# Optimization experiments

Measured on AMD Instinct MI355X. Metric: run time of the kernel, lower is better.

The kernel has to match this reference:

```python
import jax, jax.numpy as jnp
import numpy as np

WIDTH = 4096
DEPTH = 512
N_HIST = 20
N_SCALES = 64
BIAS_SCALE = 1.0


def setup_inputs() -> dict:
    key = jax.random.key(0)
    k1, k2, k3, k4, k5 = jax.random.split(key, 5)
    x = jax.random.normal(k1, (WIDTH,), dtype=jnp.float32)
    biases = jax.random.normal(k2, (DEPTH, WIDTH), dtype=jnp.float32)
    W = jax.random.normal(k3, (WIDTH, WIDTH), dtype=jnp.float32)          # linop.Random matrix
    W_bias = jax.random.normal(k4, (WIDTH, WIDTH), dtype=jnp.float32)
    weight_scales = jax.random.uniform(k5, (N_SCALES,), dtype=jnp.float32)
    return {"x": x, "biases": biases, "W": W, "W_bias": W_bias,
            "weight_scales": weight_scales}


def reference(x, biases, W, W_bias, weight_scales):
    """forward_parallel of Network (mode='rand', no residual, no normalize).

    Returns (n_scales, n_hist, width): last n_hist states of a depth-unrolled
    reservoir: curr <- erf(s * (curr @ W^T) + bias) / sqrt(width).
    """
    inv_sqrt_w = np.float32(1.0 / np.sqrt(WIDTH))
    # biases = einsum('ij,nj->ni', W_bias, biases): (depth, width)
    b = jnp.einsum('ij,nj->ni', W_bias, biases)
    curr0 = jnp.tile(x[None, :], (N_SCALES, 1))  # (n_scales, width)

    def step(curr, bi):
        pre = weight_scales[:, None] * (curr @ W.T) + BIAS_SCALE * bi[None, :]
        nxt = jax.scipy.special.erf(pre) * inv_sqrt_w
        return nxt, nxt

    _, states = jax.lax.scan(step, curr0, b)       # (depth, n_scales, width)
    out = jnp.transpose(states[-N_HIST:], (1, 0, 2))  # (n_scales, n_hist, width)
    return out
```

## Files before the change

### kernel.cpp

```cpp
#include <hip/hip_runtime.h>
#include <cstdint>
#include <cstddef>

#define WIDTH 4096
#define DEPTH 512
#define NHIST 20
#define NWG 256
#define NTHR 1024

typedef __attribute__((ext_vector_type(4))) float f32x4;
typedef __attribute__((ext_vector_type(8))) short bf16x8;

__device__ __forceinline__ ushort f2bf(float f) {
    uint32_t u = __float_as_uint(f);
    u += 0x7FFFu + ((u >> 16) & 1u);
    return (ushort)(u >> 16);
}


__global__ __launch_bounds__(256) void init_curr_kernel(const float* __restrict__ x,
                                                        ushort* __restrict__ cur) {
    int g = blockIdx.x * 256 + threadIdx.x;
    int kv = g >> 6, m = g & 63;
    int unit = ((kv >> 2) * 4 + (m >> 4)) * 64 + (kv & 3) * 16 + (m & 15);
    ushort4 lo, hi;
    lo.x = f2bf(x[kv * 8 + 0]); lo.y = f2bf(x[kv * 8 + 1]);
    lo.z = f2bf(x[kv * 8 + 2]); lo.w = f2bf(x[kv * 8 + 3]);
    hi.x = f2bf(x[kv * 8 + 4]); hi.y = f2bf(x[kv * 8 + 5]);
    hi.z = f2bf(x[kv * 8 + 6]); hi.w = f2bf(x[kv * 8 + 7]);
    ushort* dst = cur + (size_t)unit * 8;
    *(ushort4*)dst = lo;
    *(ushort4*)(dst + 4) = hi;
}

__global__ __launch_bounds__(256) void zero_flags_kernel(int* __restrict__ flags) {
    flags[blockIdx.x * 256 + threadIdx.x] = 0;
}

__global__ __launch_bounds__(256) void bias_gemm_kernel(const float* __restrict__ A,
                                                        const float* __restrict__ B,
                                                        float* __restrict__ C) {
    __shared__ float As[64][36];
    __shared__ float Bs[64][36];
    const int bm = blockIdx.y;
    const int bn = blockIdx.x;
    const int t  = threadIdx.x;
    const int tx = t & 15, ty = t >> 4;
    const int lr = t >> 3;
    const int lc = (t & 7) * 4;

    float acc[4][4] = {};
    for (int k0 = 0; k0 < WIDTH; k0 += 32) {
        float4 a0 = *(const float4*)&A[(size_t)(bm * 64 + lr) * WIDTH + k0 + lc];
        float4 a1 = *(const float4*)&A[(size_t)(bm * 64 + lr + 32) * WIDTH + k0 + lc];
        float4 b0 = *(const float4*)&B[(size_t)(bn * 64 + lr) * WIDTH + k0 + lc];
        float4 b1 = *(const float4*)&B[(size_t)(bn * 64 + lr + 32) * WIDTH + k0 + lc];
        __syncthreads();
        *(float4*)&As[lr][lc] = a0;  *(float4*)&As[lr + 32][lc] = a1;
        *(float4*)&Bs[lr][lc] = b0;  *(float4*)&Bs[lr + 32][lc] = b1;
        __syncthreads();
        #pragma unroll
        for (int k = 0; k < 32; k += 4) {
            float4 av[4], bv[4];
            #pragma unroll
            for (int mi = 0; mi < 4; mi++) av[mi] = *(const float4*)&As[ty * 4 + mi][k];
            #pragma unroll
            for (int ni = 0; ni < 4; ni++) bv[ni] = *(const float4*)&Bs[tx * 4 + ni][k];
            #pragma unroll
            for (int mi = 0; mi < 4; mi++)
                #pragma unroll
                for (int ni = 0; ni < 4; ni++)
                    acc[mi][ni] += av[mi].x * bv[ni].x + av[mi].y * bv[ni].y +
                                   av[mi].z * bv[ni].z + av[mi].w * bv[ni].w;
        }
    }
    #pragma unroll
    for (int mi = 0; mi < 4; mi++) {
        float4 v = make_float4(acc[mi][0], acc[mi][1], acc[mi][2], acc[mi][3]);
        *(float4*)&C[(size_t)(bm * 64 + ty * 4 + mi) * WIDTH + bn * 64 + tx * 4] = v;
    }
}

__global__ __launch_bounds__(NTHR, 4) void reservoir_kernel(
    const float* __restrict__ W,
    const float* __restrict__ scales,
    const float* __restrict__ b,
    float* __restrict__ out,
    ushort* __restrict__ cur0,
    ushort* __restrict__ cur1,
    int* __restrict__ flags)
{
    __shared__ float partial[16 * 32 * 32];
    __shared__ float vals[32 * 33];

    const int tid  = threadIdx.x;
    const int w    = tid >> 6;
    const int lane = tid & 63;
    const int lrow = lane & 15;
    const int lq   = lane >> 4;
    const int t    = blockIdx.x;
    const int c0   = (t >> 1) * 32;
    const int r0   = (t & 1) * 32;
    const int mb0  = (t & 1) * 2;
    int* gflag = flags + 4096;

    const int ecol = tid >> 5;
    const int erow = tid & 31;
    const float sc_e = scales[r0 + erow];

    bf16x8 wf[2][8];
    #pragma unroll
    for (int nb = 0; nb < 2; nb++) {
        #pragma unroll
        for (int kc = 0; kc < 8; kc++) {
            const float* src = W + (size_t)(c0 + nb * 16 + lrow) * WIDTH + w * 256 + kc * 32 + lq * 8;
            float4 f0 = *(const float4*)src;
            float4 f1 = *(const float4*)(src + 4);
            bf16x8 v;
            v[0] = (short)f2bf(f0.x); v[1] = (short)f2bf(f0.y);
            v[2] = (short)f2bf(f0.z); v[3] = (short)f2bf(f0.w);
            v[4] = (short)f2bf(f1.x); v[5] = (short)f2bf(f1.y);
            v[6] = (short)f2bf(f1.z); v[7] = (short)f2bf(f1.w);
            wf[nb][kc] = v;
        }
    }

    ushort* curs[2] = {cur0, cur1};

    for (int d = 0; d < DEPTH; d++) {
        if (d > 0) {
            if (tid == 0) {
                while (__hip_atomic_load(gflag, __ATOMIC_RELAXED, __HIP_MEMORY_SCOPE_AGENT) < d)
                    __builtin_amdgcn_s_sleep(1);
                (void)__hip_atomic_load(gflag, __ATOMIC_ACQUIRE, __HIP_MEMORY_SCOPE_AGENT);
            }
            __syncthreads();
        }

        const ushort* cin  = curs[d & 1];
        ushort*       cout = curs[(d + 1) & 1];
        const float bv = b[(size_t)d * WIDTH + c0 + ecol];

        f32x4 acc[2][2];
        #pragma unroll
        for (int i = 0; i < 2; i++)
            #pragma unroll
            for (int nb = 0; nb < 2; nb++)
                acc[i][nb] = (f32x4){0.f, 0.f, 0.f, 0.f};

        const ushort* abase = cin + (size_t)w * 16384 + ((size_t)lq * 16 + lrow) * 8;
        bf16x8 afA[2], afB[2];
        #pragma unroll
        for (int i = 0; i < 2; i++)
            afA[i] = *(const bf16x8*)(abase + (size_t)(mb0 + i) * 512);

        #pragma unroll
        for (int kc = 0; kc < 8; kc += 2) {
            #pragma unroll
            for (int i = 0; i < 2; i++)
                afB[i] = *(const bf16x8*)(abase + ((size_t)(kc + 1) * 4 + mb0 + i) * 512);
            #pragma unroll
            for (int i = 0; i < 2; i++) {
                acc[i][0] = __builtin_amdgcn_mfma_f32_16x16x32_bf16(afA[i], wf[0][kc], acc[i][0], 0, 0, 0);
                acc[i][1] = __builtin_amdgcn_mfma_f32_16x16x32_bf16(afA[i], wf[1][kc], acc[i][1], 0, 0, 0);
            }
            if (kc + 2 < 8) {
                #pragma unroll
                for (int i = 0; i < 2; i++)
                    afA[i] = *(const bf16x8*)(abase + ((size_t)(kc + 2) * 4 + mb0 + i) * 512);
            }
            #pragma unroll
            for (int i = 0; i < 2; i++) {
                acc[i][0] = __builtin_amdgcn_mfma_f32_16x16x32_bf16(afB[i], wf[0][kc + 1], acc[i][0], 0, 0, 0);
                acc[i][1] = __builtin_amdgcn_mfma_f32_16x16x32_bf16(afB[i], wf[1][kc + 1], acc[i][1], 0, 0, 0);
            }
        }

        #pragma unroll
        for (int i = 0; i < 2; i++) {
            #pragma unroll
            for (int nb = 0; nb < 2; nb++) {
                const int col   = nb * 16 + lrow;
                const int rbase = (i * 16 + lq * 4) ^ ((lrow & 7) << 2);
                *(f32x4*)&partial[w * 1024 + col * 32 + rbase] = acc[i][nb];
            }
        }
        __syncthreads();

        {
            const int swz = erow ^ ((ecol & 7) << 2);
            const float* p = &partial[ecol * 32 + swz];
            float s0 = 0.f, s1 = 0.f, s2 = 0.f, s3 = 0.f;
            #pragma unroll
            for (int ww = 0; ww < 16; ww += 4) {
                s0 += p[(ww + 0) * 1024];
                s1 += p[(ww + 1) * 1024];
                s2 += p[(ww + 2) * 1024];
                s3 += p[(ww + 3) * 1024];
            }
            const float sum = (s0 + s1) + (s2 + s3);
            vals[ecol * 33 + erow] = erff(sc_e * sum + bv) * 0.015625f;
        }
        __syncthreads();

        if (tid < 256) {
            const int ml   = tid & 31;
            const int kvl  = (tid >> 5) & 3;
            const int half = tid >> 7;
            const int cb   = kvl * 8 + half * 4;
            const int m    = r0 + ml;
            const int kv   = (c0 >> 3) + kvl;
            uint64_t pack =
                 (uint64_t)f2bf(vals[(cb + 0) * 33 + ml])
               | ((uint64_t)f2bf(vals[(cb + 1) * 33 + ml]) << 16)
               | ((uint64_t)f2bf(vals[(cb + 2) * 33 + ml]) << 32)
               | ((uint64_t)f2bf(vals[(cb + 3) * 33 + ml]) << 48);
            int unit = ((kv >> 2) * 4 + (m >> 4)) * 64 + (kv & 3) * 16 + (m & 15);
            uint64_t* dst = (uint64_t*)(cout + (size_t)unit * 8 + half * 4);
            __hip_atomic_store(dst, pack, __ATOMIC_RELAXED, __HIP_MEMORY_SCOPE_AGENT);
        }

        const int h = d - (DEPTH - NHIST);
        if (h >= 0 && tid < 512) {
            const int ml = tid >> 4;
            const int c  = (tid & 15) * 2;
            union { uint64_t u; float f[2]; } p;
            p.f[0] = vals[(c + 0) * 33 + ml];
            p.f[1] = vals[(c + 1) * 33 + ml];
            uint64_t* dst = (uint64_t*)(out + ((size_t)(r0 + ml) * NHIST + h) * WIDTH + c0 + c);
            __hip_atomic_store(dst, p.u, __ATOMIC_RELAXED, __HIP_MEMORY_SCOPE_AGENT);
        }

        __syncthreads();
        if (tid == 0)
            __hip_atomic_store(flags + t * 16, d + 1,
                               __ATOMIC_RELEASE, __HIP_MEMORY_SCOPE_AGENT);

        if (t == 0 && w == 0) {
            for (;;) {
                bool ok = true;
                #pragma unroll
                for (int q = 0; q < 4; q++) {
                    int v = __hip_atomic_load(flags + (lane * 4 + q) * 16,
                                              __ATOMIC_RELAXED, __HIP_MEMORY_SCOPE_AGENT);
                    ok = ok && (v >= d + 1);
                }
                if (__all(ok)) break;
                __builtin_amdgcn_s_sleep(1);
            }
            if (lane == 0) {
                (void)__hip_atomic_load(flags, __ATOMIC_ACQUIRE, __HIP_MEMORY_SCOPE_AGENT);
                __hip_atomic_store(gflag, d + 1, __ATOMIC_RELEASE, __HIP_MEMORY_SCOPE_AGENT);
            }
        }
    }
}

extern "C" void kernel_launch(void* const* d_in, const int* in_sizes, int n_in,
                              void* d_out, int out_size, void* d_ws, size_t ws_size,
                              hipStream_t stream) {
    const float* x      = (const float*)d_in[0];
    const float* biases = (const float*)d_in[1];
    const float* W      = (const float*)d_in[2];
    const float* W_bias = (const float*)d_in[3];
    const float* scales = (const float*)d_in[4];
    float* out = (float*)d_out;

    char* ws = (char*)d_ws;
    float*  b    = (float*)ws;
    ushort* cur0 = (ushort*)(ws + ((size_t)8 << 20));
    ushort* cur1 = (ushort*)(ws + ((size_t)8 << 20) + (512 << 10));
    int*    flags = (int*)(ws + ((size_t)9 << 20));

    init_curr_kernel<<<128, 256, 0, stream>>>(x, cur0);
    zero_flags_kernel<<<32, 256, 0, stream>>>(flags);
    bias_gemm_kernel<<<dim3(64, 8), 256, 0, stream>>>(biases, W_bias, b);

    void* args[] = {(void*)&W, (void*)&scales, (void*)&b, (void*)&out,
                    (void*)&cur0, (void*)&cur1, (void*)&flags};
    hipLaunchCooperativeKernel((const void*)reservoir_kernel, dim3(NWG), dim3(NTHR),
                               args, 0, stream);
}
```

Measured before the change: 5.543 ms.

## Speculatively prefetch next-step activation chunks from blocks that already published

Each wave polls the per-block flags of the producer blocks for its first four K chunks. For chunks whose producers have already finished, it loads the next step's bf16 activations before the global barrier, using relaxed atomic loads. The per-block flag store moves earlier, ahead of the history-output writes, and the MFMA loop is restructured to consume the prefetched fragments first. This hides part of the global-load latency after the grid-wide sync, at the cost of extra flag polling, more registers for the prefetch buffers, and reliance on relaxed ordering being correct for the early reads.

```diff
diff --git a/kernel.cpp b/kernel.cpp
--- a/kernel.cpp
+++ b/kernel.cpp
@@ -104,6 +104,8 @@
     const int mb0  = (t & 1) * 2;
     int* gflag = flags + 4096;
 
+    const int* pflag = flags + (((w * 8 + (lane & 7)) * 2 + (t & 1)) * 16);
+
     const int ecol = tid >> 5;
     const int erow = tid & 31;
     const float sc_e = scales[r0 + erow];
@@ -127,6 +129,9 @@
 
     ushort* curs[2] = {cur0, cur1};
 
+    bf16x8 pre[4][2];
+    unsigned int rdy = 0;
+
     for (int d = 0; d < DEPTH; d++) {
         if (d > 0) {
             if (tid == 0) {
@@ -141,6 +146,16 @@
         ushort*       cout = curs[(d + 1) & 1];
         const float bv = b[(size_t)d * WIDTH + c0 + ecol];
 
+        const ushort* abase = cin + (size_t)w * 16384 + ((size_t)lq * 16 + lrow) * 8;
+
+        #pragma unroll
+        for (int kc = 0; kc < 4; kc++) {
+            if (!((rdy >> kc) & 1u)) {
+                pre[kc][0] = *(const bf16x8*)(abase + ((size_t)kc * 4 + mb0) * 512);
+                pre[kc][1] = *(const bf16x8*)(abase + ((size_t)kc * 4 + mb0 + 1) * 512);
+            }
+        }
+
         f32x4 acc[2][2];
         #pragma unroll
         for (int i = 0; i < 2; i++)
@@ -148,32 +163,47 @@
             for (int nb = 0; nb < 2; nb++)
                 acc[i][nb] = (f32x4){0.f, 0.f, 0.f, 0.f};
 
-        const ushort* abase = cin + (size_t)w * 16384 + ((size_t)lq * 16 + lrow) * 8;
         bf16x8 afA[2], afB[2];
         #pragma unroll
         for (int i = 0; i < 2; i++)
-            afA[i] = *(const bf16x8*)(abase + (size_t)(mb0 + i) * 512);
-
-        #pragma unroll
-        for (int kc = 0; kc < 8; kc += 2) {
-            #pragma unroll
-            for (int i = 0; i < 2; i++)
-                afB[i] = *(const bf16x8*)(abase + ((size_t)(kc + 1) * 4 + mb0 + i) * 512);
+            afA[i] = *(const bf16x8*)(abase + ((size_t)16 + mb0 + i) * 512);
+        #pragma unroll
+        for (int i = 0; i < 2; i++)
+            afB[i] = *(const bf16x8*)(abase + ((size_t)20 + mb0 + i) * 512);
+
+        #pragma unroll
+        for (int kc = 0; kc < 4; kc++) {
             #pragma unroll
             for (int i = 0; i < 2; i++) {
-                acc[i][0] = __builtin_amdgcn_mfma_f32_16x16x32_bf16(afA[i], wf[0][kc], acc[i][0], 0, 0, 0);
-                acc[i][1] = __builtin_amdgcn_mfma_f32_16x16x32_bf16(afA[i], wf[1][kc], acc[i][1], 0, 0, 0);
-            }
-            if (kc + 2 < 8) {
-                #pragma unroll
-                for (int i = 0; i < 2; i++)
-                    afA[i] = *(const bf16x8*)(abase + ((size_t)(kc + 2) * 4 + mb0 + i) * 512);
-            }
-            #pragma unroll
-            for (int i = 0; i < 2; i++) {
-                acc[i][0] = __builtin_amdgcn_mfma_f32_16x16x32_bf16(afB[i], wf[0][kc + 1], acc[i][0], 0, 0, 0);
-                acc[i][1] = __builtin_amdgcn_mfma_f32_16x16x32_bf16(afB[i], wf[1][kc + 1], acc[i][1], 0, 0, 0);
-            }
+                acc[i][0] = __builtin_amdgcn_mfma_f32_16x16x32_bf16(pre[kc][i], wf[0][kc], acc[i][0], 0, 0, 0);
+                acc[i][1] = __builtin_amdgcn_mfma_f32_16x16x32_bf16(pre[kc][i], wf[1][kc], acc[i][1], 0, 0, 0);
+            }
+        }
+        #pragma unroll
+        for (int i = 0; i < 2; i++) {
+            acc[i][0] = __builtin_amdgcn_mfma_f32_16x16x32_bf16(afA[i], wf[0][4], acc[i][0], 0, 0, 0);
+            acc[i][1] = __builtin_amdgcn_mfma_f32_16x16x32_bf16(afA[i], wf[1][4], acc[i][1], 0, 0, 0);
+        }
+        #pragma unroll
+        for (int i = 0; i < 2; i++)
+            afA[i] = *(const bf16x8*)(abase + ((size_t)24 + mb0 + i) * 512);
+        #pragma unroll
+        for (int i = 0; i < 2; i++) {
+            acc[i][0] = __builtin_amdgcn_mfma_f32_16x16x32_bf16(afB[i], wf[0][5], acc[i][0], 0, 0, 0);
+            acc[i][1] = __builtin_amdgcn_mfma_f32_16x16x32_bf16(afB[i], wf[1][5], acc[i][1], 0, 0, 0);
+        }
+        #pragma unroll
+        for (int i = 0; i < 2; i++)
+            afB[i] = *(const bf16x8*)(abase + ((size_t)28 + mb0 + i) * 512);
+        #pragma unroll
+        for (int i = 0; i < 2; i++) {
+            acc[i][0] = __builtin_amdgcn_mfma_f32_16x16x32_bf16(afA[i], wf[0][6], acc[i][0], 0, 0, 0);
+            acc[i][1] = __builtin_amdgcn_mfma_f32_16x16x32_bf16(afA[i], wf[1][6], acc[i][1], 0, 0, 0);
+        }
+        #pragma unroll
+        for (int i = 0; i < 2; i++) {
+            acc[i][0] = __builtin_amdgcn_mfma_f32_16x16x32_bf16(afB[i], wf[0][7], acc[i][0], 0, 0, 0);
+            acc[i][1] = __builtin_amdgcn_mfma_f32_16x16x32_bf16(afB[i], wf[1][7], acc[i][1], 0, 0, 0);
         }
 
         #pragma unroll
@@ -220,6 +250,35 @@
             __hip_atomic_store(dst, pack, __ATOMIC_RELAXED, __HIP_MEMORY_SCOPE_AGENT);
         }
 
+        __syncthreads();
+        if (tid == 0)
+            __hip_atomic_store(flags + t * 16, d + 1,
+                               __ATOMIC_RELEASE, __HIP_MEMORY_SCOPE_AGENT);
+
+        if (d + 1 < DEPTH) {
+            int pv = __hip_atomic_load(pflag, __ATOMIC_RELAXED, __HIP_MEMORY_SCOPE_AGENT);
+            unsigned long long bal = __ballot(pv >= d + 1);
+            const ushort* nbase = cout + (size_t)w * 16384 + ((size_t)lq * 16 + lrow) * 8;
+            rdy = 0;
+            #pragma unroll
+            for (int kc = 0; kc < 4; kc++) {
+                if ((bal >> kc) & 1ull) {
+                    const ushort* p0 = nbase + ((size_t)kc * 4 + mb0) * 512;
+                    const ushort* p1 = nbase + ((size_t)kc * 4 + mb0 + 1) * 512;
+                    union { unsigned long long u[2]; bf16x8 v; } fa, fb;
+                    fa.u[0] = __hip_atomic_load((const unsigned long long*)p0,       __ATOMIC_RELAXED, __HIP_MEMORY_SCOPE_AGENT);
+                    fa.u[1] = __hip_atomic_load((const unsigned long long*)(p0 + 4), __ATOMIC_RELAXED, __HIP_MEMORY_SCOPE_AGENT);
+                    fb.u[0] = __hip_atomic_load((const unsigned long long*)p1,       __ATOMIC_RELAXED, __HIP_MEMORY_SCOPE_AGENT);
+                    fb.u[1] = __hip_atomic_load((const unsigned long long*)(p1 + 4), __ATOMIC_RELAXED, __HIP_MEMORY_SCOPE_AGENT);
+                    pre[kc][0] = fa.v;
+                    pre[kc][1] = fb.v;
+                    rdy |= (1u << kc);
+                }
+            }
+        } else {
+            rdy = 0;
+        }
+
         const int h = d - (DEPTH - NHIST);
         if (h >= 0 && tid < 512) {
             const int ml = tid >> 4;
@@ -230,11 +289,6 @@
             uint64_t* dst = (uint64_t*)(out + ((size_t)(r0 + ml) * NHIST + h) * WIDTH + c0 + c);
             __hip_atomic_store(dst, p.u, __ATOMIC_RELAXED, __HIP_MEMORY_SCOPE_AGENT);
         }
-
-        __syncthreads();
-        if (tid == 0)
-            __hip_atomic_store(flags + t * 16, d + 1,
-                               __ATOMIC_RELEASE, __HIP_MEMORY_SCOPE_AGENT);
 
         if (t == 0 && w == 0) {
             for (;;) {
```

Result: slower. 6.812 ms (+22.9%).
